# Performance work log

Measured on AMD Instinct MI355X. Metric: run time of the kernel, lower is better.

The kernel has to match this reference:

```python
import jax, jax.numpy as jnp
import numpy as np

N_SAMPLES = 32768          # exp.n_samples = 2**15
TABLE_SIZE = 4096          # table_size init arg
STD = 0.01                 # hard-coded std fill in forward
WIN_EPS = 1e-8             # Window epsilon added to std
NORM_EPS = 1e-8            # max_norm epsilon (repo convention)


def setup_inputs() -> dict:
    key = jax.random.key(0)
    k1, k2 = jax.random.split(key)
    x = jax.random.normal(k1, (1, 1, N_SAMPLES), dtype=jnp.float32)        # unused by forward
    f0 = jax.random.uniform(k2, (1, 1), dtype=jnp.float32)                 # nn.Parameter uniform(0,1)
    table = jnp.sin(jnp.linspace(-np.pi, np.pi, TABLE_SIZE, dtype=jnp.float32))[None, :]  # (1, T)
    return {"x": x, "f0": f0, "table": table, "n_samples": N_SAMPLES}


def reference(x, f0, table, n_samples):
    table_size = table.shape[1]
    sigma = STD + WIN_EPS
    # phase accumulator: cumsum of constant |f0|, wrapped to [0, 1)
    f0a = jnp.abs(f0)                                                       # (1, 1)
    pos = jnp.mod(jnp.cumsum(jnp.broadcast_to(f0a, (1, n_samples)), axis=-1), 1.0)  # (1, N)
    mu = pos[:, :, None]                                                    # (1, N, 1); mn=0, scale=1
    rng = jnp.linspace(0.0, 1.0, table_size, dtype=x.dtype)[None, None, :]  # (1, 1, T)
    # Normal(mu, sigma).log_prob(rng), exponentiated -> Gaussian pdf windows
    log_norm = jnp.float32(-np.log(sigma) - 0.5 * np.log(2.0 * np.pi))
    z = (rng - mu) / sigma                                                  # (1, N, T) large intermediate
    windows = jnp.exp(-0.5 * z * z + log_norm)
    # max_norm: per-row normalize by max abs
    windows = windows / (jnp.max(jnp.abs(windows), axis=-1, keepdims=True) + NORM_EPS)
    # windows @ table.T : soft wavetable lookup reduction
    sig = jnp.einsum('bnt,ot->bno', windows, table)                         # (1, N, 1)
    return sig.reshape(1, 1, n_samples)
```

## Files before the change

kernel.cpp:

```cpp
#include <hip/hip_runtime.h>


#define NS   32768
#define TS   4096
#define BLK  256
#define LPS  8
#define SPB  (BLK / LPS)
#define NBLK (NS / SPB)
#define HALF 176
#define NCHUNK 88
#define TPAD 4352

__global__ __launch_bounds__(BLK) void wt_kernel(const float* __restrict__ f0p,
                                                 const float* __restrict__ table,
                                                 float* __restrict__ out)
{
    __shared__ float tab[TPAD];
    const int tid = threadIdx.x;
    {
        const float4* t4 = (const float4*)table;
        float4* s4 = (float4*)tab;
        #pragma unroll
        for (int i = tid; i < TS / 4; i += BLK) s4[i] = t4[i];
        for (int i = TS / 4 + tid; i < TPAD / 4; i += BLK)
            s4[i] = make_float4(0.f, 0.f, 0.f, 0.f);
    }
    const float f0a = fabsf(f0p[0]);
    __syncthreads();

    const int g = blockIdx.x * BLK + tid;
    const int n = g >> 3;
    const int j = g & (LPS - 1);

    const double sigma = 0.01 + 1e-8;
    const float  log_norm = 3.6862306527839187f;

    const double mu = fmod((double)(n + 1) * (double)f0a, 1.0);

    const int tc = (int)(mu * 4095.0 + 0.5);
    const float zsf = (float)(((double)tc * (1.0 / 4095.0) - mu) / sigma);
    const float peak = __expf(fmaf(-0.5f * zsf, zsf, log_norm));
    const float denom = peak + 1e-8f;

    int t0 = tc - HALF;
    t0 = (t0 < 0) ? 0 : t0;
    t0 &= ~3;

    const float dz = (float)(1.0 / (4095.0 * sigma));
    const float z0 = (float)(((double)t0 * (1.0 / 4095.0) - mu) / sigma);

    const float4* __restrict__ src = (const float4*)(tab + t0);
    float acc = 0.f;
    #pragma unroll
    for (int c = j; c < NCHUNK; c += LPS) {
        const float4 v = src[c];
        const float e0 = (float)(4 * c);
        float z;
        z = fmaf(e0,        dz, z0); acc = fmaf(__expf(fmaf(-0.5f * z, z, log_norm)), v.x, acc);
        z = fmaf(e0 + 1.f,  dz, z0); acc = fmaf(__expf(fmaf(-0.5f * z, z, log_norm)), v.y, acc);
        z = fmaf(e0 + 2.f,  dz, z0); acc = fmaf(__expf(fmaf(-0.5f * z, z, log_norm)), v.z, acc);
        z = fmaf(e0 + 3.f,  dz, z0); acc = fmaf(__expf(fmaf(-0.5f * z, z, log_norm)), v.w, acc);
    }

    acc += __shfl_xor(acc, 1);
    acc += __shfl_xor(acc, 2);
    acc += __shfl_xor(acc, 4);
    if (j == 0) out[n] = acc / denom;
}

extern "C" void kernel_launch(void* const* d_in, const int* in_sizes, int n_in,
                              void* d_out, int out_size, void* d_ws, size_t ws_size,
                              hipStream_t stream)
{
    const float* f0    = (const float*)d_in[1];
    const float* table = (const float*)d_in[2];
    float* out = (float*)d_out;
    wt_kernel<<<dim3(NBLK), dim3(BLK), 0, stream>>>(f0, table, out);
}
```

Baseline: 9.931 us.

## Factor Gaussian window into precomputed table times geometric ratio recurrence

Rewrites exp(-0.5*(z0+k*dz)^2) as exp(-0.5 z0^2) * exp(-z0*dz*k) * exp(-0.5 dz^2 k^2). The k^2 part is precomputed once per block into shared memory, and the linear part is carried as a running product, so the per-tap exp calls become multiplies. It also narrows the window half-width from 176 to 144 taps. The intent is to cut transcendental work in the inner loop. In exchange it adds an extra shared load per chunk and risks overflow or underflow and accumulated rounding error in the ratio recurrence.

After: 9.595 us (median of 2 runs). 1.03x faster.

```diff
diff --git a/kernel.cpp b/kernel.cpp
--- a/kernel.cpp
+++ b/kernel.cpp
@@ -1,22 +1,30 @@
 #include <hip/hip_runtime.h>
 
 
-#define NS   32768
-#define TS   4096
-#define BLK  256
-#define LPS  8
-#define SPB  (BLK / LPS)
-#define NBLK (NS / SPB)
-#define HALF 176
-#define NCHUNK 88
-#define TPAD 4352
+#define NS     32768
+#define TS     4096
+#define BLK    256
+#define LPS    8
+#define SPB    (BLK / LPS)
+#define NBLK   (NS / SPB)
+#define HALF   144
+#define NCHUNK 72
+#define NTAP   (NCHUNK * 4)
+#define TPAD   4352
 
 __global__ __launch_bounds__(BLK) void wt_kernel(const float* __restrict__ f0p,
                                                  const float* __restrict__ table,
                                                  float* __restrict__ out)
 {
-    __shared__ float tab[TPAD];
+    __shared__ __align__(16) float tab[TPAD];
+    __shared__ __align__(16) float gtab[NTAP];
     const int tid = threadIdx.x;
+
+    constexpr double SIGMA = 0.01 + 1e-8;
+    constexpr double DZ    = 1.0 / (4095.0 * SIGMA);
+    constexpr float  GC    = (float)(-0.5 * DZ * DZ);
+    const float log_norm = 3.6862306527839187f;
+
     {
         const float4* t4 = (const float4*)table;
         float4* s4 = (float4*)tab;
@@ -24,6 +32,10 @@
         for (int i = tid; i < TS / 4; i += BLK) s4[i] = t4[i];
         for (int i = TS / 4 + tid; i < TPAD / 4; i += BLK)
             s4[i] = make_float4(0.f, 0.f, 0.f, 0.f);
+        for (int k = tid; k < NTAP; k += BLK) {
+            const float kf = (float)k;
+            gtab[k] = __expf(GC * kf * kf);
+        }
     }
     const float f0a = fabsf(f0p[0]);
     __syncthreads();
@@ -32,13 +44,10 @@
     const int n = g >> 3;
     const int j = g & (LPS - 1);
 
-    const double sigma = 0.01 + 1e-8;
-    const float  log_norm = 3.6862306527839187f;
-
     const double mu = fmod((double)(n + 1) * (double)f0a, 1.0);
 
     const int tc = (int)(mu * 4095.0 + 0.5);
-    const float zsf = (float)(((double)tc * (1.0 / 4095.0) - mu) / sigma);
+    const float zsf = (float)(((double)tc * (1.0 / 4095.0) - mu) / SIGMA);
     const float peak = __expf(fmaf(-0.5f * zsf, zsf, log_norm));
     const float denom = peak + 1e-8f;
 
@@ -46,26 +55,36 @@
     t0 = (t0 < 0) ? 0 : t0;
     t0 &= ~3;
 
-    const float dz = (float)(1.0 / (4095.0 * sigma));
-    const float z0 = (float)(((double)t0 * (1.0 / 4095.0) - mu) / sigma);
+    const double z0d = ((double)t0 * (1.0 / 4095.0) - mu) / SIGMA;
+    const float  z0  = (float)z0d;
+    const float  bb  = (float)(-z0d * DZ);
+
+    const float e0  = __expf(fmaf(-0.5f * z0, z0, log_norm));
+    const float r1  = __expf(bb);
+    const float r32 = __expf(bb * 32.0f);
+    float       rk  = __expf(bb * (float)(4 * j));
+    const float r2  = r1 * r1;
+    const float r3  = r2 * r1;
 
     const float4* __restrict__ src = (const float4*)(tab + t0);
+    const float4* __restrict__ gsrc = (const float4*)gtab;
     float acc = 0.f;
     #pragma unroll
     for (int c = j; c < NCHUNK; c += LPS) {
-        const float4 v = src[c];
-        const float e0 = (float)(4 * c);
-        float z;
-        z = fmaf(e0,        dz, z0); acc = fmaf(__expf(fmaf(-0.5f * z, z, log_norm)), v.x, acc);
-        z = fmaf(e0 + 1.f,  dz, z0); acc = fmaf(__expf(fmaf(-0.5f * z, z, log_norm)), v.y, acc);
-        z = fmaf(e0 + 2.f,  dz, z0); acc = fmaf(__expf(fmaf(-0.5f * z, z, log_norm)), v.z, acc);
-        z = fmaf(e0 + 3.f,  dz, z0); acc = fmaf(__expf(fmaf(-0.5f * z, z, log_norm)), v.w, acc);
+        const float4 v  = src[c];
+        const float4 gg = gsrc[c];
+        const float w1 = rk * r1, w2 = rk * r2, w3 = rk * r3;
+        acc = fmaf(rk * gg.x, v.x, acc);
+        acc = fmaf(w1 * gg.y, v.y, acc);
+        acc = fmaf(w2 * gg.z, v.z, acc);
+        acc = fmaf(w3 * gg.w, v.w, acc);
+        rk *= r32;
     }
 
     acc += __shfl_xor(acc, 1);
     acc += __shfl_xor(acc, 2);
     acc += __shfl_xor(acc, 4);
-    if (j == 0) out[n] = acc / denom;
+    if (j == 0) out[n] = acc * e0 / denom;
 }
 
 extern "C" void kernel_launch(void* const* d_in, const int* in_sizes, int n_in,
```
